# Kernel optimization log

Hardware: AMD Instinct MI355X
Metric: run time of the kernel (lower is better)

The kernel has to match this reference:

```python
import jax, jax.numpy as jnp
import numpy as np

D_MODEL = 1024
N_HEAD = 16
EPS = 1e-11  # non-standard: masked scores are set to eps BEFORE softmax (not -inf)


def setup_inputs() -> dict:
    key = jax.random.key(0)
    ks = jax.random.split(key, 12)
    B, S, D = 4, 2048, D_MODEL
    s = 1.0 / np.sqrt(D)
    return {
        "query": jax.random.normal(ks[0], (B, S, D), dtype=jnp.float32),
        "key": jax.random.normal(ks[1], (B, S, D), dtype=jnp.float32),
        "value": jax.random.normal(ks[2], (B, S, D), dtype=jnp.float32),
        "mask": jax.random.randint(ks[3], (B, S, S), 0, 2, dtype=jnp.int32),
        "wq": jax.random.normal(ks[4], (D, D), dtype=jnp.float32) * s,
        "bq": jnp.zeros((D,), dtype=jnp.float32),
        "wk": jax.random.normal(ks[5], (D, D), dtype=jnp.float32) * s,
        "bk": jnp.zeros((D,), dtype=jnp.float32),
        "wv": jax.random.normal(ks[6], (D, D), dtype=jnp.float32) * s,
        "bv": jnp.zeros((D,), dtype=jnp.float32),
        "wo": jax.random.normal(ks[7], (D, D), dtype=jnp.float32) * s,
        "bo": jnp.zeros((D,), dtype=jnp.float32),
    }


def reference(query, key, value, mask, wq, bq, wk, bk, wv, bv, wo, bo):
    B, S, D = query.shape
    H = N_HEAD
    dk = D // H
    # QKV projections (nn.Linear: x @ W.T + b)
    q = query @ wq.T + bq
    k = key @ wk.T + bk
    v = value @ wv.T + bv
    # [B, S, D] -> [B, H, S, dk]
    q = q.reshape(B, S, H, dk).transpose(0, 2, 1, 3)
    k = k.reshape(B, S, H, dk).transpose(0, 2, 1, 3)
    v = v.reshape(B, S, H, dk).transpose(0, 2, 1, 3)
    # scaled dot-product scores [B, H, S, S]
    scores = jnp.einsum("bhqd,bhkd->bhqk", q, k) / jnp.sqrt(jnp.float32(dk))
    # faithful quirk: fill masked positions with eps (not -inf)
    m = mask[:, None, :, :]  # [B, 1, S, S]
    scores = jnp.where(m == 0, jnp.float32(EPS), scores)
    attn = jax.nn.softmax(scores, axis=-1)
    out = jnp.einsum("bhqk,bhkd->bhqd", attn, v)
    out = out.transpose(0, 2, 1, 3).reshape(B, S, D)
    return out @ wo.T + bo
```

## Files before the change

### kernel.cpp

```cpp
#include <hip/hip_runtime.h>

typedef __attribute__((ext_vector_type(8))) short short8;
typedef __attribute__((ext_vector_type(4))) float floatx4;

__device__ inline unsigned short f2bf(float f) {
    union { float f; unsigned int i; } c; c.f = f;
    unsigned int x = c.i;
    unsigned int r = x + 0x7fffu + ((x >> 16) & 1u);
    return (unsigned short)(r >> 16);
}

__device__ inline unsigned int pk_bf16(float lo, float hi) {
#if __has_builtin(__builtin_amdgcn_cvt_pk_bf16_f32)
    auto pk = __builtin_amdgcn_cvt_pk_bf16_f32(lo, hi);
    return __builtin_bit_cast(unsigned int, pk);
#else
    return (unsigned int)f2bf(lo) | ((unsigned int)f2bf(hi) << 16);
#endif
}

__device__ inline void gl_lds16(const unsigned short* g, unsigned short* lds_uniform) {
    __builtin_amdgcn_global_load_lds(
        (const __attribute__((address_space(1))) void*)g,
        (__attribute__((address_space(3))) void*)lds_uniform,
        16, 0, 0);
}

__global__ void cvt_bf16(const float* __restrict__ in, unsigned short* __restrict__ out, int n8)
{
    int i = blockIdx.x * blockDim.x + threadIdx.x;
    if (i < n8) {
        const float4* p = (const float4*)(in + (size_t)i * 8);
        float4 a = p[0], b = p[1];
        short8 v;
        v[0] = (short)f2bf(a.x); v[1] = (short)f2bf(a.y);
        v[2] = (short)f2bf(a.z); v[3] = (short)f2bf(a.w);
        v[4] = (short)f2bf(b.x); v[5] = (short)f2bf(b.y);
        v[6] = (short)f2bf(b.z); v[7] = (short)f2bf(b.w);
        *(short8*)(out + (size_t)i * 8) = v;
    }
}

__global__ void mask_pack(const int* __restrict__ m, unsigned short* __restrict__ o, int n16)
{
    int i = blockIdx.x * blockDim.x + threadIdx.x;
    if (i < n16) {
        const int4* p = (const int4*)(m + (size_t)i * 16);
        unsigned int bits = 0;
#pragma unroll
        for (int j = 0; j < 4; j++) {
            int4 v = p[j];
            bits |= (v.x != 0 ? 1u : 0u) << (j * 4 + 0);
            bits |= (v.y != 0 ? 1u : 0u) << (j * 4 + 1);
            bits |= (v.z != 0 ? 1u : 0u) << (j * 4 + 2);
            bits |= (v.w != 0 ? 1u : 0u) << (j * 4 + 3);
        }
        o[i] = (unsigned short)bits;
    }
}

__global__ __launch_bounds__(256, 2)
void gemm_bt(const unsigned short* __restrict__ A,
             const unsigned short* __restrict__ W,
             const float* __restrict__ bias,
             void* __restrict__ outv,
             int M, int N, int K, int mode)
{
    __shared__ __align__(16) unsigned short As[128 * 64];
    __shared__ __align__(16) unsigned short Bs[128 * 64];
    const int t = threadIdx.x, lane = t & 63, wv = t >> 6;
    const int quad = lane >> 4, l16 = lane & 15;
    const int m0 = blockIdx.x * 128, n0 = blockIdx.y * 128;
    const int wm = (wv >> 1) * 64, wn = (wv & 1) * 64;

    floatx4 acc[4][4] = {};

    for (int k0 = 0; k0 < K; k0 += 64) {
#pragma unroll
        for (int s = 0; s < 4; s++) {
            int e = t + s * 256;
            int row = e >> 3, slot = e & 7;
            int chunk = slot ^ (row & 7);
            gl_lds16(&A[(size_t)(m0 + row) * K + k0 + chunk * 8], &As[wv * 512 + s * 2048]);
            gl_lds16(&W[(size_t)(n0 + row) * K + k0 + chunk * 8], &Bs[wv * 512 + s * 2048]);
        }
        asm volatile("s_waitcnt vmcnt(0)" ::: "memory");
        __syncthreads();

        short8 af[4][2], bfr[4][2];
#pragma unroll
        for (int i = 0; i < 4; i++)
#pragma unroll
            for (int c = 0; c < 2; c++)
                af[i][c] = *(const short8*)&As[(wm + i * 16 + l16) * 64 + (((c * 4 + quad) ^ (l16 & 7)) * 8)];
#pragma unroll
        for (int j = 0; j < 4; j++)
#pragma unroll
            for (int c = 0; c < 2; c++)
                bfr[j][c] = *(const short8*)&Bs[(wn + j * 16 + l16) * 64 + (((c * 4 + quad) ^ (l16 & 7)) * 8)];

#pragma unroll
        for (int c = 0; c < 2; c++)
#pragma unroll
            for (int i = 0; i < 4; i++)
#pragma unroll
                for (int j = 0; j < 4; j++)
                    acc[i][j] = __builtin_amdgcn_mfma_f32_16x16x32_bf16(af[i][c], bfr[j][c], acc[i][j], 0, 0, 0);
        __syncthreads();
    }

#pragma unroll
    for (int i = 0; i < 4; i++) {
#pragma unroll
        for (int j = 0; j < 4; j++) {
            int n = n0 + wn + j * 16 + l16;
            float bv = bias[n];
#pragma unroll
            for (int r = 0; r < 4; r++) {
                int m = m0 + wm + i * 16 + quad * 4 + r;
                float v = acc[i][j][r] + bv;
                if (mode == 2) {
                    ((float*)outv)[(size_t)m * N + n] = v;
                } else {
                    int b = m >> 11, s = m & 2047, h = n >> 6, d = n & 63;
                    size_t idx = (mode == 0)
                        ? (((size_t)b * 16 + h) * 2048 + s) * 64 + d
                        : (((size_t)b * 16 + h) * 64 + d) * 2048 + s;
                    ((unsigned short*)outv)[idx] = f2bf(v);
                }
            }
        }
    }
}

__global__ __launch_bounds__(256, 4)
void attn(const unsigned short* __restrict__ qb,
          const unsigned short* __restrict__ kb,
          const unsigned short* __restrict__ vtb,
          const unsigned char* __restrict__ mb,
          unsigned short* __restrict__ ob)
{
    __shared__ __align__(16) unsigned short Ks[64 * 64];
    __shared__ __align__(16) unsigned short Vs[64 * 64];
    __shared__ __align__(16) unsigned short Ps[4][2][16][72];
    const int t = threadIdx.x, lane = t & 63, wv = t >> 6;
    const int quad = lane >> 4, l16 = lane & 15;
    const int bh = blockIdx.x & 63;
    const int b = bh >> 4, h = bh & 15;
    const int q0 = (blockIdx.x >> 6) * 128;
    const size_t kvbase = (size_t)bh * 2048 * 64;
    const float K1 = 0.1803368801e0f;
    const float K2 = -14.4269504089f;
    const float PM = 4.5399931e-05f;

    short8 aq[2][2];
#pragma unroll
    for (int mi = 0; mi < 2; mi++)
#pragma unroll
        for (int c = 0; c < 2; c++)
            aq[mi][c] = *(const short8*)&qb[kvbase + (size_t)(q0 + wv * 32 + mi * 16 + l16) * 64 + c * 32 + quad * 8];

    floatx4 O[2][4] = {};
    float lrun[2][4] = {};

    for (int kt0 = 0; kt0 < 2048; kt0 += 64) {
#pragma unroll
        for (int s = 0; s < 2; s++) {
            int e = t + s * 256;
            int row = e >> 3, slot = e & 7;
            int chunk = slot ^ (row & 7);
            gl_lds16(&kb[kvbase + (size_t)(kt0 + row) * 64 + chunk * 8], &Ks[wv * 512 + s * 2048]);
            gl_lds16(&vtb[kvbase + (size_t)row * 2048 + kt0 + chunk * 8], &Vs[wv * 512 + s * 2048]);
        }
        asm volatile("s_waitcnt vmcnt(0)" ::: "memory");
        __syncthreads();

        short8 bk[4][2];
#pragma unroll
        for (int j = 0; j < 4; j++)
#pragma unroll
            for (int c = 0; c < 2; c++)
                bk[j][c] = *(const short8*)&Ks[(j * 16 + l16) * 64 + (((c * 4 + quad) ^ (l16 & 7)) * 8)];

#pragma unroll
        for (int mi = 0; mi < 2; mi++) {
            floatx4 sc[4];
#pragma unroll
            for (int j = 0; j < 4; j++) {
                floatx4 z = {0.f, 0.f, 0.f, 0.f};
                z = __builtin_amdgcn_mfma_f32_16x16x32_bf16(aq[mi][0], bk[j][0], z, 0, 0, 0);
                z = __builtin_amdgcn_mfma_f32_16x16x32_bf16(aq[mi][1], bk[j][1], z, 0, 0, 0);
                sc[j] = z;
            }
            float rsum[4];
#pragma unroll
            for (int r = 0; r < 4; r++) {
                int qr = q0 + wv * 32 + mi * 16 + quad * 4 + r;
                uint2 mrow = *(const uint2*)(mb + ((size_t)b * 2048 + qr) * 256 + (kt0 >> 3));
                float p[4];
                float acc_r = 0.f;
#pragma unroll
                for (int j = 0; j < 4; j++) {
                    unsigned int w = (j < 2) ? mrow.x : mrow.y;
                    unsigned int bit = (w >> ((j & 1) * 16 + l16)) & 1u;
                    float e_ = exp2f(fmaf(sc[j][r], K1, K2));
                    p[j] = bit ? e_ : PM;
                    acc_r += p[j];
                }
                rsum[r] = acc_r;
                unsigned int pk01 = pk_bf16(p[0], p[1]);
                unsigned int pk23 = pk_bf16(p[2], p[3]);
                unsigned short* prow = &Ps[wv][mi][quad * 4 + r][l16];
                prow[0]  = (unsigned short)pk01;
                prow[16] = (unsigned short)(pk01 >> 16);
                prow[32] = (unsigned short)pk23;
                prow[48] = (unsigned short)(pk23 >> 16);
            }
#pragma unroll
            for (int r = 0; r < 4; r++) {
                float s_ = rsum[r];
                s_ += __shfl_xor(s_, 1, 64);
                s_ += __shfl_xor(s_, 2, 64);
                s_ += __shfl_xor(s_, 4, 64);
                s_ += __shfl_xor(s_, 8, 64);
                lrun[mi][r] += s_;
            }
        }

        short8 bv[4][2];
#pragma unroll
        for (int j = 0; j < 4; j++)
#pragma unroll
            for (int c = 0; c < 2; c++)
                bv[j][c] = *(const short8*)&Vs[(j * 16 + l16) * 64 + (((c * 4 + quad) ^ (l16 & 7)) * 8)];
#pragma unroll
        for (int mi = 0; mi < 2; mi++) {
            short8 ap[2];
#pragma unroll
            for (int c = 0; c < 2; c++)
                ap[c] = *(const short8*)&Ps[wv][mi][l16][c * 32 + quad * 8];
#pragma unroll
            for (int j = 0; j < 4; j++) {
                O[mi][j] = __builtin_amdgcn_mfma_f32_16x16x32_bf16(ap[0], bv[j][0], O[mi][j], 0, 0, 0);
                O[mi][j] = __builtin_amdgcn_mfma_f32_16x16x32_bf16(ap[1], bv[j][1], O[mi][j], 0, 0, 0);
            }
        }
        __syncthreads();
    }

#pragma unroll
    for (int mi = 0; mi < 2; mi++)
#pragma unroll
        for (int j = 0; j < 4; j++)
#pragma unroll
            for (int r = 0; r < 4; r++) {
                int qr = q0 + wv * 32 + mi * 16 + quad * 4 + r;
                float v = O[mi][j][r] / lrun[mi][r];
                ob[((size_t)b * 2048 + qr) * 1024 + h * 64 + j * 16 + l16] = f2bf(v);
            }
}

extern "C" void kernel_launch(void* const* d_in, const int* in_sizes, int n_in,
                              void* d_out, int out_size, void* d_ws, size_t ws_size,
                              hipStream_t stream)
{
    const float* query = (const float*)d_in[0];
    const float* key   = (const float*)d_in[1];
    const float* value = (const float*)d_in[2];
    const int*   mask  = (const int*)d_in[3];
    const float* wq = (const float*)d_in[4];
    const float* bq = (const float*)d_in[5];
    const float* wk = (const float*)d_in[6];
    const float* bk = (const float*)d_in[7];
    const float* wv = (const float*)d_in[8];
    const float* bv = (const float*)d_in[9];
    const float* wo = (const float*)d_in[10];
    const float* bo = (const float*)d_in[11];

    char* ws = (char*)d_ws;
    const size_t T = 16777216;
    unsigned short* S0 = (unsigned short*)(ws);
    unsigned short* S1 = (unsigned short*)(ws + T);
    unsigned short* S2 = (unsigned short*)(ws + 2 * T);
    unsigned short* D0 = (unsigned short*)d_out;
    unsigned short* D1 = (unsigned short*)((char*)d_out + T);

    dim3 g(64, 8);

    cvt_bf16<<<dim3(4096), 256, 0, stream>>>(query, S0, 1048576);
    cvt_bf16<<<dim3(512),  256, 0, stream>>>(wq, D1, 131072);
    gemm_bt<<<g, 256, 0, stream>>>(S0, D1, bq, S1, 8192, 1024, 1024, 0);
    cvt_bf16<<<dim3(4096), 256, 0, stream>>>(key, S0, 1048576);
    cvt_bf16<<<dim3(512),  256, 0, stream>>>(wk, D1, 131072);
    gemm_bt<<<g, 256, 0, stream>>>(S0, D1, bk, S2, 8192, 1024, 1024, 0);
    cvt_bf16<<<dim3(4096), 256, 0, stream>>>(value, S0, 1048576);
    cvt_bf16<<<dim3(512),  256, 0, stream>>>(wv, D1, 131072);
    gemm_bt<<<g, 256, 0, stream>>>(S0, D1, bv, D0, 8192, 1024, 1024, 1);

    mask_pack<<<dim3(4096), 256, 0, stream>>>(mask, D1, 1048576);

    attn<<<dim3(1024), 256, 0, stream>>>(S1, S2, D0, (const unsigned char*)D1, S0);

    cvt_bf16<<<dim3(512), 256, 0, stream>>>(wo, S1, 131072);
    gemm_bt<<<g, 256, 0, stream>>>(S0, S1, bo, d_out, 8192, 1024, 1024, 2);
}
```

Before: 528.1 us.

## Rework attention kernel with transposed 32x32 MFMA, register-resident P, and double-buffered K/V

The attention kernel now computes S^T = K·Q^T with 32x32x16 bf16 MFMAs, so each lane owns one query row. That removes the cross-lane row-sum shuffles, and permlane32 swaps let P feed the PV MFMA straight from registers with no LDS round-trip. K/V tiles are double-buffered in LDS so the next tile's global-to-LDS loads overlap compute, and the mask words are prefetched one tile ahead. Output is written as packed bf16 pairs. In exchange it doubles K/V LDS use and raises register pressure (floatx16 accumulators, p[16]), which may reduce occupancy under launch_bounds(256,4).

Measured after the change: 474.1 us. -10.2%, faster.

```diff
diff --git a/kernel.cpp b/kernel.cpp
--- a/kernel.cpp
+++ b/kernel.cpp
@@ -2,6 +2,8 @@
 
 typedef __attribute__((ext_vector_type(8))) short short8;
 typedef __attribute__((ext_vector_type(4))) float floatx4;
+typedef __attribute__((ext_vector_type(16))) float floatx16;
+typedef __attribute__((ext_vector_type(4))) unsigned int uintx4;
 
 __device__ inline unsigned short f2bf(float f) {
     union { float f; unsigned int i; } c; c.f = f;
@@ -11,11 +13,22 @@
 }
 
 __device__ inline unsigned int pk_bf16(float lo, float hi) {
-#if __has_builtin(__builtin_amdgcn_cvt_pk_bf16_f32)
-    auto pk = __builtin_amdgcn_cvt_pk_bf16_f32(lo, hi);
-    return __builtin_bit_cast(unsigned int, pk);
+    unsigned int r;
+    asm("v_cvt_pk_bf16_f32 %0, %1, %2" : "=v"(r) : "v"(lo), "v"(hi));
+    return r;
+}
+
+__device__ inline void plane_swap(unsigned int& a, unsigned int& b) {
+#if __has_builtin(__builtin_amdgcn_permlane32_swap)
+    auto r = __builtin_amdgcn_permlane32_swap(a, b, false, false);
+    a = r[0]; b = r[1];
 #else
-    return (unsigned int)f2bf(lo) | ((unsigned int)f2bf(hi) << 16);
+    int lane = threadIdx.x & 63;
+    unsigned int tb = (unsigned int)__shfl_xor((int)b, 32, 64);
+    unsigned int ta = (unsigned int)__shfl_xor((int)a, 32, 64);
+    unsigned int na = (lane < 32) ? a : tb;
+    unsigned int nb = (lane < 32) ? ta : b;
+    a = na; b = nb;
 #endif
 }
 
@@ -140,124 +153,116 @@
           const unsigned char* __restrict__ mb,
           unsigned short* __restrict__ ob)
 {
-    __shared__ __align__(16) unsigned short Ks[64 * 64];
-    __shared__ __align__(16) unsigned short Vs[64 * 64];
-    __shared__ __align__(16) unsigned short Ps[4][2][16][72];
+    __shared__ __align__(16) unsigned short Ks[2][64 * 64];
+    __shared__ __align__(16) unsigned short Vs[2][64 * 64];
     const int t = threadIdx.x, lane = t & 63, wv = t >> 6;
-    const int quad = lane >> 4, l16 = lane & 15;
+    const int hi = lane >> 5, l31 = lane & 31;
     const int bh = blockIdx.x & 63;
     const int b = bh >> 4, h = bh & 15;
     const int q0 = (blockIdx.x >> 6) * 128;
     const size_t kvbase = (size_t)bh * 2048 * 64;
-    const float K1 = 0.1803368801e0f;
+    const float K1 = 0.1803368801f;
     const float K2 = -14.4269504089f;
     const float PM = 4.5399931e-05f;
 
-    short8 aq[2][2];
-#pragma unroll
-    for (int mi = 0; mi < 2; mi++)
-#pragma unroll
-        for (int c = 0; c < 2; c++)
-            aq[mi][c] = *(const short8*)&qb[kvbase + (size_t)(q0 + wv * 32 + mi * 16 + l16) * 64 + c * 32 + quad * 8];
-
-    floatx4 O[2][4] = {};
-    float lrun[2][4] = {};
-
-    for (int kt0 = 0; kt0 < 2048; kt0 += 64) {
-#pragma unroll
-        for (int s = 0; s < 2; s++) {
-            int e = t + s * 256;
-            int row = e >> 3, slot = e & 7;
-            int chunk = slot ^ (row & 7);
-            gl_lds16(&kb[kvbase + (size_t)(kt0 + row) * 64 + chunk * 8], &Ks[wv * 512 + s * 2048]);
-            gl_lds16(&vtb[kvbase + (size_t)row * 2048 + kt0 + chunk * 8], &Vs[wv * 512 + s * 2048]);
-        }
+    const int qr = q0 + wv * 32 + l31;
+
+    short8 qf[4];
+#pragma unroll
+    for (int g = 0; g < 4; g++)
+        qf[g] = *(const short8*)&qb[kvbase + (size_t)qr * 64 + g * 16 + hi * 8];
+
+    const uint2* mrowp = (const uint2*)(mb + ((size_t)b * 2048 + qr) * 256);
+    uint2 mcur = mrowp[0];
+
+    floatx16 O[2] = {};
+    float lrun = 0.f;
+
+#pragma unroll
+    for (int s = 0; s < 2; s++) {
+        int e = t + s * 256;
+        int row = e >> 3, slot = e & 7, chunk = slot ^ (row & 7);
+        gl_lds16(&kb[kvbase + (size_t)row * 64 + chunk * 8], &Ks[0][wv * 512 + s * 2048]);
+        gl_lds16(&vtb[kvbase + (size_t)row * 2048 + chunk * 8], &Vs[0][wv * 512 + s * 2048]);
+    }
+
+    for (int kt = 0; kt < 2048; kt += 64) {
+        const int cur = (kt >> 6) & 1;
         asm volatile("s_waitcnt vmcnt(0)" ::: "memory");
         __syncthreads();
 
-        short8 bk[4][2];
-#pragma unroll
-        for (int j = 0; j < 4; j++)
-#pragma unroll
-            for (int c = 0; c < 2; c++)
-                bk[j][c] = *(const short8*)&Ks[(j * 16 + l16) * 64 + (((c * 4 + quad) ^ (l16 & 7)) * 8)];
-
-#pragma unroll
-        for (int mi = 0; mi < 2; mi++) {
-            floatx4 sc[4];
-#pragma unroll
-            for (int j = 0; j < 4; j++) {
-                floatx4 z = {0.f, 0.f, 0.f, 0.f};
-                z = __builtin_amdgcn_mfma_f32_16x16x32_bf16(aq[mi][0], bk[j][0], z, 0, 0, 0);
-                z = __builtin_amdgcn_mfma_f32_16x16x32_bf16(aq[mi][1], bk[j][1], z, 0, 0, 0);
-                sc[j] = z;
+        uint2 mnext = mcur;
+        if (kt + 64 < 2048) {
+#pragma unroll
+            for (int s = 0; s < 2; s++) {
+                int e = t + s * 256;
+                int row = e >> 3, slot = e & 7, chunk = slot ^ (row & 7);
+                gl_lds16(&kb[kvbase + (size_t)(kt + 64 + row) * 64 + chunk * 8],
+                         &Ks[cur ^ 1][wv * 512 + s * 2048]);
+                gl_lds16(&vtb[kvbase + (size_t)row * 2048 + (kt + 64) + chunk * 8],
+                         &Vs[cur ^ 1][wv * 512 + s * 2048]);
             }
-            float rsum[4];
-#pragma unroll
-            for (int r = 0; r < 4; r++) {
-                int qr = q0 + wv * 32 + mi * 16 + quad * 4 + r;
-                uint2 mrow = *(const uint2*)(mb + ((size_t)b * 2048 + qr) * 256 + (kt0 >> 3));
-                float p[4];
-                float acc_r = 0.f;
-#pragma unroll
-                for (int j = 0; j < 4; j++) {
-                    unsigned int w = (j < 2) ? mrow.x : mrow.y;
-                    unsigned int bit = (w >> ((j & 1) * 16 + l16)) & 1u;
-                    float e_ = exp2f(fmaf(sc[j][r], K1, K2));
-                    p[j] = bit ? e_ : PM;
-                    acc_r += p[j];
-                }
-                rsum[r] = acc_r;
-                unsigned int pk01 = pk_bf16(p[0], p[1]);
-                unsigned int pk23 = pk_bf16(p[2], p[3]);
-                unsigned short* prow = &Ps[wv][mi][quad * 4 + r][l16];
-                prow[0]  = (unsigned short)pk01;
-                prow[16] = (unsigned short)(pk01 >> 16);
-                prow[32] = (unsigned short)pk23;
-                prow[48] = (unsigned short)(pk23 >> 16);
+            mnext = mrowp[(kt >> 6) + 1];
+        }
+
+#pragma unroll
+        for (int c32 = 0; c32 < 2; c32++) {
+            const int krow = c32 * 32 + l31;
+            short8 kf[4];
+#pragma unroll
+            for (int g = 0; g < 4; g++)
+                kf[g] = *(const short8*)&Ks[cur][krow * 64 + (((g * 2 + hi) ^ (krow & 7)) * 8)];
+
+            floatx16 C = {};
+#pragma unroll
+            for (int g = 0; g < 4; g++)
+                C = __builtin_amdgcn_mfma_f32_32x32x16_bf16(kf[g], qf[g], C, 0, 0, 0);
+
+            unsigned int w = (c32 ? mcur.y : mcur.x) >> (hi * 4);
+            float p[16];
+            float rs = 0.f;
+#pragma unroll
+            for (int r = 0; r < 16; r++) {
+                float e_ = exp2f(fmaf(C[r], K1, K2));
+                unsigned int bit = (w >> ((r & 3) + 8 * (r >> 2))) & 1u;
+                p[r] = bit ? e_ : PM;
+                rs += p[r];
             }
-#pragma unroll
-            for (int r = 0; r < 4; r++) {
-                float s_ = rsum[r];
-                s_ += __shfl_xor(s_, 1, 64);
-                s_ += __shfl_xor(s_, 2, 64);
-                s_ += __shfl_xor(s_, 4, 64);
-                s_ += __shfl_xor(s_, 8, 64);
-                lrun[mi][r] += s_;
+            lrun += rs;
+
+            unsigned int s_[8];
+#pragma unroll
+            for (int i = 0; i < 8; i++) s_[i] = pk_bf16(p[2 * i], p[2 * i + 1]);
+            plane_swap(s_[0], s_[2]); plane_swap(s_[1], s_[3]);
+            plane_swap(s_[4], s_[6]); plane_swap(s_[5], s_[7]);
+            short8 fragA = __builtin_bit_cast(short8, (uintx4){s_[0], s_[1], s_[2], s_[3]});
+            short8 fragB = __builtin_bit_cast(short8, (uintx4){s_[4], s_[5], s_[6], s_[7]});
+
+#pragma unroll
+            for (int dt = 0; dt < 2; dt++) {
+                const int vrow = dt * 32 + l31;
+                short8 vA = *(const short8*)&Vs[cur][vrow * 64 + (((c32 * 4 + hi) ^ (vrow & 7)) * 8)];
+                short8 vB = *(const short8*)&Vs[cur][vrow * 64 + (((c32 * 4 + 2 + hi) ^ (vrow & 7)) * 8)];
+                O[dt] = __builtin_amdgcn_mfma_f32_32x32x16_bf16(vA, fragA, O[dt], 0, 0, 0);
+                O[dt] = __builtin_amdgcn_mfma_f32_32x32x16_bf16(vB, fragB, O[dt], 0, 0, 0);
             }
         }
-
-        short8 bv[4][2];
-#pragma unroll
-        for (int j = 0; j < 4; j++)
-#pragma unroll
-            for (int c = 0; c < 2; c++)
-                bv[j][c] = *(const short8*)&Vs[(j * 16 + l16) * 64 + (((c * 4 + quad) ^ (l16 & 7)) * 8)];
-#pragma unroll
-        for (int mi = 0; mi < 2; mi++) {
-            short8 ap[2];
-#pragma unroll
-            for (int c = 0; c < 2; c++)
-                ap[c] = *(const short8*)&Ps[wv][mi][l16][c * 32 + quad * 8];
-#pragma unroll
-            for (int j = 0; j < 4; j++) {
-                O[mi][j] = __builtin_amdgcn_mfma_f32_16x16x32_bf16(ap[0], bv[j][0], O[mi][j], 0, 0, 0);
-                O[mi][j] = __builtin_amdgcn_mfma_f32_16x16x32_bf16(ap[1], bv[j][1], O[mi][j], 0, 0, 0);
-            }
-        }
+        mcur = mnext;
         __syncthreads();
     }
 
-#pragma unroll
-    for (int mi = 0; mi < 2; mi++)
-#pragma unroll
-        for (int j = 0; j < 4; j++)
-#pragma unroll
-            for (int r = 0; r < 4; r++) {
-                int qr = q0 + wv * 32 + mi * 16 + quad * 4 + r;
-                float v = O[mi][j][r] / lrun[mi][r];
-                ob[((size_t)b * 2048 + qr) * 1024 + h * 64 + j * 16 + l16] = f2bf(v);
-            }
+    float l = lrun + __shfl_xor(lrun, 32, 64);
+    float inv = 1.0f / l;
+#pragma unroll
+    for (int dt = 0; dt < 2; dt++)
+#pragma unroll
+        for (int g = 0; g < 4; g++) {
+            int d0 = dt * 32 + 8 * g + 4 * hi;
+            unsigned int w0 = pk_bf16(O[dt][4 * g + 0] * inv, O[dt][4 * g + 1] * inv);
+            unsigned int w1 = pk_bf16(O[dt][4 * g + 2] * inv, O[dt][4 * g + 3] * inv);
+            uint2 ww; ww.x = w0; ww.y = w1;
+            *(uint2*)&ob[((size_t)b * 2048 + qr) * 1024 + h * 64 + d0] = ww;
+        }
 }
 
 extern "C" void kernel_launch(void* const* d_in, const int* in_sizes, int n_in,
```
